# Performance work log

Hardware: AMD Instinct MI355X
Metric: run time of the kernel (lower is better)

Reference implementation:

```python
import jax, jax.numpy as jnp
import numpy as np

VOCAB, XS, HS, NCLASS = 32000, 256, 256, 2
B, DEPTH = 128, 9
NTREE = 2 ** (DEPTH + 1) - 1  # 1023 nodes per perfect binary tree


def setup_inputs() -> dict:
    key = jax.random.key(0)
    ks = jax.random.split(key, 10)
    return {
        'types1': jax.random.randint(ks[0], (B, NTREE), 0, VOCAB, dtype=jnp.int32),
        'types2': jax.random.randint(ks[1], (B, NTREE), 0, VOCAB, dtype=jnp.int32),
        'emb': jax.random.normal(ks[2], (VOCAB, XS), jnp.float32) * 0.1,
        'W_iou': jax.random.normal(ks[3], (3 * HS, XS), jnp.float32) * 0.05,
        'U_iou': jax.random.normal(ks[4], (3 * HS, HS), jnp.float32) * 0.05,
        'b_iou': jnp.zeros((1, 3 * HS), jnp.float32),
        'U_f_w': jax.random.normal(ks[5], (HS, HS), jnp.float32) * 0.05,
        'U_f_b': jnp.zeros((HS,), jnp.float32),
        'cls_w': jax.random.normal(ks[6], (NCLASS, HS), jnp.float32) * 0.05,
        'cls_b': jnp.zeros((NCLASS,), jnp.float32),
    }


def _tree_forward(types, emb, W_iou, U_iou, b_iou, U_f_w, U_f_b):
    # types: [B, NTREE] heap layout (node j has children 2j+1, 2j+2)
    x = emb[types]                       # [B, N, XS] embedding gather
    wx = x @ W_iou.T                     # [B, N, 3H] leaf iou (DGL reduce overwrites it for internal nodes)
    h = jnp.zeros((types.shape[0], NTREE, HS), wx.dtype)
    c = jnp.zeros_like(h)
    for lvl in range(DEPTH, -1, -1):     # bottom-up topological levels (static)
        idx = np.arange(2 ** lvl - 1, 2 ** (lvl + 1) - 1)
        if lvl == DEPTH:  # leaves: no mailbox, keep W_iou(x)
            iou = wx[:, idx] + b_iou
            c_sum = 0.0
        else:
            ch = np.stack([2 * idx + 1, 2 * idx + 2], axis=-1)  # [n, 2]
            h_ch = h[:, ch]              # [B, n, 2, H] child mailbox
            c_ch = c[:, ch]
            h_tild = h_ch.sum(axis=2)
            f = jax.nn.sigmoid(h_ch @ U_f_w.T + U_f_b)
            c_sum = (f * c_ch).sum(axis=2)
            iou = h_tild @ U_iou.T + b_iou  # overwrites wx per DGL semantics
        i, o, u = jnp.split(iou, 3, axis=-1)
        c_new = jax.nn.sigmoid(i) * jnp.tanh(u) + c_sum
        h_new = jax.nn.sigmoid(o) * jnp.tanh(c_new)
        h = h.at[:, idx].set(h_new)
        c = c.at[:, idx].set(c_new)
    return h.mean(axis=1)                # AvgPooling over nodes -> [B, H]


def reference(types1, types2, emb, W_iou, U_iou, b_iou, U_f_w, U_f_b, cls_w, cls_b):
    rep1 = _tree_forward(types1, emb, W_iou, U_iou, b_iou, U_f_w, U_f_b)
    rep2 = _tree_forward(types2, emb, W_iou, U_iou, b_iou, U_f_w, U_f_b)
    return jnp.abs(rep1 - rep2) @ cls_w.T + cls_b  # [B, NCLASS]
```

## Files before the change

kernel.cpp:

```cpp
#include <hip/hip_runtime.h>
#include <math.h>


typedef _Float16 h16;
typedef h16 f16x8 __attribute__((ext_vector_type(8)));
typedef h16 h16x4 __attribute__((ext_vector_type(4)));
typedef float f32x4 __attribute__((ext_vector_type(4)));

#define HS 256
#define NTREE 1023
#define B2 256

#define DMA16(gp, lp) __builtin_amdgcn_global_load_lds( \
    (const __attribute__((address_space(1))) void*)(gp), \
    (__attribute__((address_space(3))) void*)(lp), 16, 0, 0)

__device__ __forceinline__ float sigf(float x){
  return __builtin_amdgcn_rcpf(1.0f + exp2f(x * -1.44269504f));
}
__device__ __forceinline__ float sig_mul_tanh(float a, float b){
  const float E1 = exp2f(a * -1.44269504f);
  const float E2 = exp2f(fminf(b * -2.88539008f, 126.0f));
  return (1.0f - E2) * __builtin_amdgcn_rcpf((1.0f + E1) * (1.0f + E2));
}

__global__ __launch_bounds__(256) void convert_all(const float* __restrict__ emb,
    const float* __restrict__ Ufw, const float* __restrict__ Uiou,
    const float* __restrict__ Wiou, h16* __restrict__ emb16,
    h16* __restrict__ W16, h16* __restrict__ Wx16, float* __restrict__ rep){
  if (blockIdx.x < 64)
    ((float4*)rep)[blockIdx.x*256 + threadIdx.x] = make_float4(0.f,0.f,0.f,0.f);
  const size_t i0 = ((size_t)blockIdx.x*256 + threadIdx.x)*8;
  const float* src; h16* dst; size_t off;
  if (i0 < 8192000UL){ src = emb;  dst = emb16;       off = i0; }
  else if (i0 < 8257536UL){ src = Ufw;  dst = W16;        off = i0 - 8192000UL; }
  else if (i0 < 8454144UL){ src = Uiou; dst = W16+65536;  off = i0 - 8257536UL; }
  else               { src = Wiou; dst = Wx16;       off = i0 - 8454144UL; }
  const float4 v0 = *(const float4*)&src[off];
  const float4 v1 = *(const float4*)&src[off+4];
  f16x8 o;
  o[0]=(h16)v0.x; o[1]=(h16)v0.y; o[2]=(h16)v0.z; o[3]=(h16)v0.w;
  o[4]=(h16)v1.x; o[5]=(h16)v1.y; o[6]=(h16)v1.z; o[7]=(h16)v1.w;
  *(f16x8*)&dst[off] = o;
}

__global__ __launch_bounds__(256) void swizzle_w(const h16* __restrict__ W16,
    h16* __restrict__ Wfrag){
  const int tid = blockIdx.x*256 + threadIdx.x;
  const int lane = tid & 63;
  const int f    = (tid >> 6) & 15;
  const int kc   = (tid >> 10) & 7;
  const int cb   = tid >> 13;
  const int g = f >> 2, cf = f & 3;
  const int row = g*256 + cb*64 + cf*16 + (lane & 15);
  const int col = kc*32 + (lane >> 4)*8;
  const f16x8 v = *(const f16x8*)&W16[(size_t)row*256 + col];
  *(f16x8*)&Wfrag[(size_t)tid*8] = v;
}

__global__ __launch_bounds__(256) void wxv_mfma(const h16* __restrict__ emb16,
    const h16* __restrict__ Wx16, h16* __restrict__ WxV){
  __shared__ h16 As[64*40];
  __shared__ h16 Bs[64*40];
  const int t = threadIdx.x, lane = t & 63, wave = t >> 6;
  const int q = lane >> 4, li = lane & 15;
  const int waveR = wave & 1, waveC = wave >> 1;
  const int bm = blockIdx.x*64, bn = blockIdx.y*64;
  const size_t aAddr = ((size_t)(bm + (t>>2)))*256 + (t&3)*8;
  const size_t bAddr = ((size_t)(bn + (t>>2)))*256 + (t&3)*8;
  const int ldsOff = (t>>2)*40 + (t&3)*8;
  f32x4 acc[2][2] = {};
  for (int k0 = 0; k0 < 256; k0 += 32){
    const f16x8 a = *(const f16x8*)&emb16[aAddr + k0];
    const f16x8 b = *(const f16x8*)&Wx16[bAddr + k0];
    __syncthreads();
    *(f16x8*)&As[ldsOff] = a;
    *(f16x8*)&Bs[ldsOff] = b;
    __syncthreads();
    #pragma unroll
    for (int rt=0; rt<2; ++rt){
      const f16x8 av = *(const f16x8*)&As[(waveR*32 + rt*16 + li)*40 + q*8];
      #pragma unroll
      for (int ct=0; ct<2; ++ct){
        const f16x8 bv = *(const f16x8*)&Bs[(waveC*32 + ct*16 + li)*40 + q*8];
        acc[rt][ct] = __builtin_amdgcn_mfma_f32_16x16x32_f16(av, bv, acc[rt][ct], 0,0,0);
      }
    }
  }
  #pragma unroll
  for (int rt=0; rt<2; ++rt)
    #pragma unroll
    for (int ct=0; ct<2; ++ct){
      const int col = bn + waveC*32 + ct*16 + li;
      #pragma unroll
      for (int reg=0; reg<4; ++reg){
        const int row = bm + waveR*32 + rt*16 + q*4 + reg;
        WxV[(size_t)row*768 + col] = (h16)acc[rt][ct][reg];
      }
    }
}

__global__ __launch_bounds__(256) void type_cell(const h16* __restrict__ WxV,
    const float* __restrict__ biou, h16* __restrict__ hT, h16* __restrict__ cT){
  const int tid = blockIdx.x*256 + threadIdx.x;
  const int row = tid >> 5;
  const int k8  = (tid & 31) * 8;
  const f16x8 vi8 = *(const f16x8*)&WxV[(size_t)row*768 + k8];
  const f16x8 vo8 = *(const f16x8*)&WxV[(size_t)row*768 + 256 + k8];
  const f16x8 vu8 = *(const f16x8*)&WxV[(size_t)row*768 + 512 + k8];
  f16x8 hO, cO;
  #pragma unroll
  for (int j=0; j<8; ++j){
    const float vi = (float)vi8[j] + biou[k8+j];
    const float vo = (float)vo8[j] + biou[256+k8+j];
    const float vu = (float)vu8[j] + biou[512+k8+j];
    const float c = sig_mul_tanh(vi, vu);
    const float h = sig_mul_tanh(vo, c);
    cO[j] = (h16)c; hO[j] = (h16)h;
  }
  *(f16x8*)&hT[(size_t)row*256 + k8] = hO;
  *(f16x8*)&cT[(size_t)row*256 + k8] = cO;
}

__global__ __launch_bounds__(256,3) void gt16_mfma(const h16* __restrict__ hT,
    const h16* __restrict__ Wfrag, const float* __restrict__ biou,
    const float* __restrict__ Ufb, h16* __restrict__ GT16){
  __shared__ h16 ldsA[4*8*64*8];
  __shared__ h16 ldsB[16*64*8];
  const int t = threadIdx.x, w = t >> 6, l = t & 63;
  const int q = l >> 4, li = l & 15;
  const int waveR = w & 1, waveC = w >> 1;
  const int bx = blockIdx.x;

  {
    const int grow = bx*64 + w*16 + li;
    const size_t abase = (size_t)grow * 256;
    #pragma unroll
    for (int kc=0; kc<8; ++kc)
      DMA16(hT + abase + kc*32 + q*8, &ldsA[(w*8 + kc)*512]);
  }

  for (int cb=0; cb<4; ++cb){
    const int colBase = cb*64;
    const h16* wfBase = Wfrag + (size_t)cb*8*16*512 + (size_t)l*8;

    #pragma unroll
    for (int i=0; i<4; ++i)
      DMA16(wfBase + ((size_t)(w*4 + i))*512, &ldsB[(w*4 + i)*512]);
    __syncthreads();

    f32x4 acc[4][2][2] = {};
    #pragma unroll
    for (int kc=0; kc<8; ++kc){
      f16x8 aF[2], bF[4][2];
      #pragma unroll
      for (int rt=0; rt<2; ++rt)
        aF[rt] = *(const f16x8*)&ldsA[(((waveR*2 + rt)*8 + kc)*64 + l)*8];
      #pragma unroll
      for (int g=0; g<4; ++g)
        #pragma unroll
        for (int ct=0; ct<2; ++ct)
          bF[g][ct] = *(const f16x8*)&ldsB[((g*4 + waveC*2 + ct)*64 + l)*8];
      __syncthreads();
      if (kc < 7){
        #pragma unroll
        for (int i=0; i<4; ++i)
          DMA16(wfBase + ((size_t)(kc+1)*16 + w*4 + i)*512,
                &ldsB[(w*4 + i)*512]);
      }
      #pragma unroll
      for (int g=0; g<4; ++g)
        #pragma unroll
        for (int rt=0; rt<2; ++rt)
          #pragma unroll
          for (int ct=0; ct<2; ++ct)
            acc[g][rt][ct] = __builtin_amdgcn_mfma_f32_16x16x32_f16(
                aF[rt], bF[g][ct], acc[g][rt][ct], 0,0,0);
      __syncthreads();
    }

    #pragma unroll
    for (int ct=0; ct<2; ++ct){
      const int c = colBase + waveC*32 + ct*16 + li;
      const float fb  = Ufb[c];
      const float bi2 = 0.5f*biou[c], bo2 = 0.5f*biou[256+c], bu2 = 0.5f*biou[512+c];
      #pragma unroll
      for (int rt=0; rt<2; ++rt){
        #pragma unroll
        for (int reg=0; reg<4; ++reg){
          const int row = bx*64 + waveR*32 + rt*16 + q*4 + reg;
          h16x4 o;
          o[0] = (h16)(acc[0][rt][ct][reg] + fb);
          o[1] = (h16)(acc[1][rt][ct][reg] + bi2);
          o[2] = (h16)(acc[2][rt][ct][reg] + bo2);
          o[3] = (h16)(acc[3][rt][ct][reg] + bu2);
          *(h16x4*)&GT16[(size_t)row*1024 + c*4] = o;
        }
      }
    }
  }
}

__global__ __launch_bounds__(256) void leaf_rep(const int* __restrict__ t1,
    const int* __restrict__ t2, const h16* __restrict__ hT,
    float* __restrict__ rep){
  const int r = blockIdx.y, jg = blockIdx.x, k = threadIdx.x;
  const int* tp = (r < 128) ? t1 : t2;
  const int b = r & 127;
  float s = 0.f;
  for (int jj=0; jj<64; ++jj){
    const int v = tp[b*NTREE + 511 + jg*64 + jj];
    s += (float)hT[(size_t)v*256 + k];
  }
  atomicAdd(&rep[r*HS + k], s);
}

__global__ __launch_bounds__(256) void lvl8_cell(const int* __restrict__ t1,
    const int* __restrict__ t2, const h16* __restrict__ GT16,
    const h16* __restrict__ cT, h16* __restrict__ hUpHigh,
    h16* __restrict__ cPar){
  const int k = threadIdx.x;
  const int m0 = blockIdx.x*32;
  #pragma unroll 4
  for (int p=0; p<32; ++p){
    const int m = m0 + p, rr = m >> 8, jn = m & 255;
    const int* tp = (rr < 128) ? t1 : t2;
    const int b = rr & 127;
    const size_t vl = (size_t)tp[b*NTREE + 511 + 2*jn];
    const size_t vr = (size_t)tp[b*NTREE + 512 + 2*jn];
    const h16x4 gl = *(const h16x4*)&GT16[vl*1024 + k*4];
    const h16x4 gr = *(const h16x4*)&GT16[vr*1024 + k*4];
    const float cl = (float)cT[vl*256 + k];
    const float cr = (float)cT[vr*256 + k];
    const float fl = sigf((float)gl[0]);
    const float fr = sigf((float)gr[0]);
    const float iv = (float)gl[1] + (float)gr[1];
    const float ov = (float)gl[2] + (float)gr[2];
    const float uv = (float)gl[3] + (float)gr[3];
    const float cnew = sig_mul_tanh(iv, uv) + fl*cl + fr*cr;
    const float hnew = sig_mul_tanh(ov, cnew);
    hUpHigh[((size_t)jn*256 + rr)*256 + k] = (h16)hnew;
    cPar[(size_t)m*256 + k] = (h16)cnew;
  }
}

__global__ __launch_bounds__(256,3) void level_mfma(
    const h16* __restrict__ hChild, const h16* __restrict__ cChild,
    const h16* __restrict__ Wfrag,
    const float* __restrict__ biou, const float* __restrict__ Ufb,
    h16* __restrict__ hUpW, h16* __restrict__ cPar,
    int log2n, int cbN, int cOff, int ndOff){
  const int n = 1 << log2n;
  const int mask2 = 2*n - 1;
  __shared__ h16 ldsA[4*8*64*8];
  __shared__ h16 ldsB[16*64*8];
  const int t = threadIdx.x, w = t >> 6, l = t & 63;
  const int q = l >> 4, li = l & 15;
  const int waveR = w & 1, waveC = w >> 1;
  const int bx = blockIdx.x;

  {
    const int grow = bx*64 + w*16 + li;
    const int cidx = grow & mask2;
    const int rr   = grow >> (log2n + 1);
    const size_t abase = ((size_t)(cOff + cidx)*256 + rr)*256;
    #pragma unroll
    for (int kc=0; kc<8; ++kc)
      DMA16(hChild + abase + kc*32 + q*8, &ldsA[(w*8 + kc)*512]);
  }

  for (int cb=0; cb<cbN; ++cb){
    const int cbi = blockIdx.y*cbN + cb;
    const int colBase = cbi*64;
    const h16* wfBase = Wfrag + (size_t)cbi*8*16*512 + (size_t)l*8;

    #pragma unroll
    for (int i=0; i<4; ++i)
      DMA16(wfBase + ((size_t)(w*4 + i))*512, &ldsB[(w*4 + i)*512]);
    __syncthreads();

    f32x4 acc[4][2][2] = {};
    #pragma unroll
    for (int kc=0; kc<8; ++kc){
      f16x8 aF[2], bF[4][2];
      #pragma unroll
      for (int rt=0; rt<2; ++rt)
        aF[rt] = *(const f16x8*)&ldsA[(((waveR*2 + rt)*8 + kc)*64 + l)*8];
      #pragma unroll
      for (int g=0; g<4; ++g)
        #pragma unroll
        for (int ct=0; ct<2; ++ct)
          bF[g][ct] = *(const f16x8*)&ldsB[((g*4 + waveC*2 + ct)*64 + l)*8];
      __syncthreads();
      if (kc < 7){
        #pragma unroll
        for (int i=0; i<4; ++i)
          DMA16(wfBase + ((size_t)(kc+1)*16 + w*4 + i)*512,
                &ldsB[(w*4 + i)*512]);
      }
      #pragma unroll
      for (int g=0; g<4; ++g)
        #pragma unroll
        for (int rt=0; rt<2; ++rt)
          #pragma unroll
          for (int ct=0; ct<2; ++ct)
            acc[g][rt][ct] = __builtin_amdgcn_mfma_f32_16x16x32_f16(
                aF[rt], bF[g][ct], acc[g][rt][ct], 0,0,0);
      __syncthreads();
    }

    #pragma unroll
    for (int ct=0; ct<2; ++ct){
      const int c = colBase + waveC*32 + ct*16 + li;
      const float fb  = Ufb[c];
      const float bi_ = biou[c], bo_ = biou[256+c], bu_ = biou[512+c];
      #pragma unroll
      for (int rt=0; rt<2; ++rt){
        #pragma unroll
        for (int pp=0; pp<2; ++pp){
          const int crel = waveR*32 + rt*16 + q*4 + 2*pp;
          const int m = bx*32 + (crel >> 1);
          const int rr2 = m >> log2n;
          const int jn = m & (n - 1);
          const float cl = (float)cChild[(size_t)(bx*64 + crel)*256 + c];
          const float cr = (float)cChild[(size_t)(bx*64 + crel + 1)*256 + c];
          const float fl = sigf(acc[0][rt][ct][2*pp]   + fb);
          const float fr = sigf(acc[0][rt][ct][2*pp+1] + fb);
          const float iv = acc[1][rt][ct][2*pp] + acc[1][rt][ct][2*pp+1] + bi_;
          const float ov = acc[2][rt][ct][2*pp] + acc[2][rt][ct][2*pp+1] + bo_;
          const float uv = acc[3][rt][ct][2*pp] + acc[3][rt][ct][2*pp+1] + bu_;
          const float cnew = sig_mul_tanh(iv, uv) + fl*cl + fr*cr;
          const float hnew = sig_mul_tanh(ov, cnew);
          hUpW[(((size_t)(ndOff + jn))*256 + rr2)*256 + c] = (h16)hnew;
          cPar[((size_t)m)*256 + c] = (h16)cnew;
        }
      }
    }
  }
}

__global__ __launch_bounds__(256) void rep_accum(const h16* __restrict__ H,
    float* __restrict__ rep, int nrows, int chunk){
  const int r = blockIdx.y, k = threadIdx.x;
  const int n0 = blockIdx.x * chunk;
  int n1 = n0 + chunk; if (n1 > nrows) n1 = nrows;
  float s = 0.f;
  for (int nd = n0; nd < n1; ++nd)
    s += (float)H[((size_t)nd*256 + r)*HS + k];
  atomicAdd(&rep[r*HS + k], s);
}

__global__ __launch_bounds__(256) void cls_kernel(const float* __restrict__ rep,
    const float* __restrict__ clsw, const float* __restrict__ clsb,
    float* __restrict__ out){
  const int b = blockIdx.x, k = threadIdx.x;
  const float d = fabsf(rep[b*HS + k] - rep[(128+b)*HS + k]) * (1.0f/1023.0f);
  __shared__ float r0[256], r1[256];
  r0[k] = d * clsw[k];
  r1[k] = d * clsw[HS + k];
  __syncthreads();
  for (int off = 128; off > 0; off >>= 1){
    if (k < off){ r0[k] += r0[k+off]; r1[k] += r1[k+off]; }
    __syncthreads();
  }
  if (k == 0){
    out[b*2 + 0] = r0[0] + clsb[0];
    out[b*2 + 1] = r1[0] + clsb[1];
  }
}

extern "C" void kernel_launch(void* const* d_in, const int* in_sizes, int n_in,
                              void* d_out, int out_size, void* d_ws, size_t ws_size,
                              hipStream_t stream){
  const int*   types1 = (const int*)d_in[0];
  const int*   types2 = (const int*)d_in[1];
  const float* emb    = (const float*)d_in[2];
  const float* Wiou   = (const float*)d_in[3];
  const float* Uiou   = (const float*)d_in[4];
  const float* biou   = (const float*)d_in[5];
  const float* Ufw    = (const float*)d_in[6];
  const float* Ufb    = (const float*)d_in[7];
  const float* clsw   = (const float*)d_in[8];
  const float* clsb   = (const float*)d_in[9];
  float* out = (float*)d_out;

  h16* ws      = (h16*)d_ws;
  h16* GT16    = ws;
  h16* WxV     = ws;
  h16* emb16   = ws + 24576000UL;
  h16* Wx16    = ws + 32768000UL;
  h16* hUpLow  = ws;
  h16* cB      = ws + 16711680UL;
  h16* hT      = ws + 65536000UL;
  h16* cT      = ws + 73728000UL;
  h16* hUpHigh = ws + 81920000UL;
  h16* cA      = ws + 98697216UL;
  h16* W16     = ws + 115474432UL;
  h16* Wfrag   = ws + 115736576UL;
  float* rep   = (float*)(ws + 116260864UL);

  convert_all<<<4224, 256, 0, stream>>>(emb, Ufw, Uiou, Wiou, emb16, W16, Wx16, rep);
  swizzle_w<<<256, 256, 0, stream>>>(W16, Wfrag);
  wxv_mfma<<<dim3(500,12), 256, 0, stream>>>(emb16, Wx16, WxV);
  type_cell<<<4000, 256, 0, stream>>>(WxV, biou, hT, cT);
  gt16_mfma<<<500, 256, 0, stream>>>(hT, Wfrag, biou, Ufb, GT16);
  leaf_rep<<<dim3(8, B2), 256, 0, stream>>>(types1, types2, hT, rep);
  lvl8_cell<<<2048, 256, 0, stream>>>(types1, types2, GT16, cT, hUpHigh, cA);

  const h16* cprev = cA;
  for (int lvl = 7; lvl >= 0; --lvl){
    const int children = 512 << lvl;
    const int cbN = (lvl >= 6) ? 4 : 1;
    h16* cout = ((8 - lvl) & 1) ? cB : cA;
    const h16* hin = (lvl == 7) ? hUpHigh : hUpLow;
    const int cOff  = (lvl == 7) ? 0 : ((1 << (lvl + 1)) - 1);
    const int ndOff = (1 << lvl) - 1;
    level_mfma<<<dim3(children/64, 4/cbN), 256, 0, stream>>>(
        hin, cprev, Wfrag, biou, Ufb, hUpLow, cout,
        lvl, cbN, cOff, ndOff);
    cprev = cout;
  }
  rep_accum<<<dim3(2, B2), 256, 0, stream>>>(hUpLow,  rep, 255, 128);
  rep_accum<<<dim3(2, B2), 256, 0, stream>>>(hUpHigh, rep, 256, 128);
  cls_kernel<<<128, 256, 0, stream>>>(rep, clsw, clsb, out);
}
```

Before: 475.2 us.

## Fuse leaf GEMM with LSTM cell, fold leaf pooling into level-8 kernel

```diff
diff --git a/kernel.cpp b/kernel.cpp
--- a/kernel.cpp
+++ b/kernel.cpp
@@ -44,82 +44,112 @@
   *(f16x8*)&dst[off] = o;
 }
 
-__global__ __launch_bounds__(256) void swizzle_w(const h16* __restrict__ W16,
-    h16* __restrict__ Wfrag){
+__global__ __launch_bounds__(256) void swizzle_all(const h16* __restrict__ W16,
+    const h16* __restrict__ Wx16, h16* __restrict__ Wfrag,
+    h16* __restrict__ WxFrag){
   const int tid = blockIdx.x*256 + threadIdx.x;
-  const int lane = tid & 63;
-  const int f    = (tid >> 6) & 15;
-  const int kc   = (tid >> 10) & 7;
-  const int cb   = tid >> 13;
-  const int g = f >> 2, cf = f & 3;
-  const int row = g*256 + cb*64 + cf*16 + (lane & 15);
-  const int col = kc*32 + (lane >> 4)*8;
-  const f16x8 v = *(const f16x8*)&W16[(size_t)row*256 + col];
-  *(f16x8*)&Wfrag[(size_t)tid*8] = v;
-}
-
-__global__ __launch_bounds__(256) void wxv_mfma(const h16* __restrict__ emb16,
-    const h16* __restrict__ Wx16, h16* __restrict__ WxV){
-  __shared__ h16 As[64*40];
-  __shared__ h16 Bs[64*40];
-  const int t = threadIdx.x, lane = t & 63, wave = t >> 6;
-  const int q = lane >> 4, li = lane & 15;
-  const int waveR = wave & 1, waveC = wave >> 1;
-  const int bm = blockIdx.x*64, bn = blockIdx.y*64;
-  const size_t aAddr = ((size_t)(bm + (t>>2)))*256 + (t&3)*8;
-  const size_t bAddr = ((size_t)(bn + (t>>2)))*256 + (t&3)*8;
-  const int ldsOff = (t>>2)*40 + (t&3)*8;
-  f32x4 acc[2][2] = {};
-  for (int k0 = 0; k0 < 256; k0 += 32){
-    const f16x8 a = *(const f16x8*)&emb16[aAddr + k0];
-    const f16x8 b = *(const f16x8*)&Wx16[bAddr + k0];
+  if (tid < 65536){
+    const int lane = tid & 63;
+    const int f    = (tid >> 6) & 15;
+    const int kc   = (tid >> 10) & 7;
+    const int cb   = tid >> 13;
+    const int g = f >> 2, cf = f & 3;
+    const int row = g*256 + cb*64 + cf*16 + (lane & 15);
+    const int col = kc*32 + (lane >> 4)*8;
+    const f16x8 v = *(const f16x8*)&W16[(size_t)row*256 + col];
+    *(f16x8*)&Wfrag[(size_t)tid*8] = v;
+  } else {
+    const int t2 = tid - 65536;
+    const int lane = t2 & 63;
+    const int frag = t2 >> 6;
+    const int cb  = frag / 96;
+    const int rem = frag % 96;
+    const int kc  = rem / 12;
+    const int f   = rem % 12;
+    const int g = f >> 2, cf = f & 3;
+    const int row = g*256 + cb*64 + cf*16 + (lane & 15);
+    const int col = kc*32 + (lane >> 4)*8;
+    const f16x8 v = *(const f16x8*)&Wx16[(size_t)row*256 + col];
+    *(f16x8*)&WxFrag[(size_t)frag*512 + lane*8] = v;
+  }
+}
+
+__global__ __launch_bounds__(256,3) void ht_mfma(const h16* __restrict__ emb16,
+    const h16* __restrict__ WxFrag, const float* __restrict__ biou,
+    h16* __restrict__ hT, h16* __restrict__ cT){
+  __shared__ h16 ldsA[4*8*64*8];
+  __shared__ h16 ldsB[12*64*8];
+  const int t = threadIdx.x, w = t >> 6, l = t & 63;
+  const int q = l >> 4, li = l & 15;
+  const int waveR = w & 1, waveC = w >> 1;
+  const int bx = blockIdx.x;
+
+  {
+    const int grow = bx*64 + w*16 + li;
+    const size_t abase = (size_t)grow * 256;
+    #pragma unroll
+    for (int kc=0; kc<8; ++kc)
+      DMA16(emb16 + abase + kc*32 + q*8, &ldsA[(w*8 + kc)*512]);
+  }
+
+  for (int cb=0; cb<4; ++cb){
+    const h16* wfBase = WxFrag + (size_t)cb*8*12*512 + (size_t)l*8;
+
+    #pragma unroll
+    for (int i=0; i<3; ++i)
+      DMA16(wfBase + ((size_t)(w*3 + i))*512, &ldsB[(w*3 + i)*512]);
     __syncthreads();
-    *(f16x8*)&As[ldsOff] = a;
-    *(f16x8*)&Bs[ldsOff] = b;
-    __syncthreads();
-    #pragma unroll
-    for (int rt=0; rt<2; ++rt){
-      const f16x8 av = *(const f16x8*)&As[(waveR*32 + rt*16 + li)*40 + q*8];
-      #pragma unroll
-      for (int ct=0; ct<2; ++ct){
-        const f16x8 bv = *(const f16x8*)&Bs[(waveC*32 + ct*16 + li)*40 + q*8];
-        acc[rt][ct] = __builtin_amdgcn_mfma_f32_16x16x32_f16(av, bv, acc[rt][ct], 0,0,0);
-      }
-    }
-  }
-  #pragma unroll
-  for (int rt=0; rt<2; ++rt)
+
+    f32x4 acc[3][2][2] = {};
+    #pragma unroll
+    for (int kc=0; kc<8; ++kc){
+      f16x8 aF[2], bF[3][2];
+      #pragma unroll
+      for (int rt=0; rt<2; ++rt)
+        aF[rt] = *(const f16x8*)&ldsA[(((waveR*2 + rt)*8 + kc)*64 + l)*8];
+      #pragma unroll
+      for (int g=0; g<3; ++g)
+        #pragma unroll
+        for (int ct=0; ct<2; ++ct)
+          bF[g][ct] = *(const f16x8*)&ldsB[((g*4 + waveC*2 + ct)*64 + l)*8];
+      __syncthreads();
+      if (kc < 7){
+        #pragma unroll
+        for (int i=0; i<3; ++i)
+          DMA16(wfBase + ((size_t)(kc+1)*12 + w*3 + i)*512,
+                &ldsB[(w*3 + i)*512]);
+      }
+      #pragma unroll
+      for (int g=0; g<3; ++g)
+        #pragma unroll
+        for (int rt=0; rt<2; ++rt)
+          #pragma unroll
+          for (int ct=0; ct<2; ++ct)
+            acc[g][rt][ct] = __builtin_amdgcn_mfma_f32_16x16x32_f16(
+                aF[rt], bF[g][ct], acc[g][rt][ct], 0,0,0);
+      __syncthreads();
+    }
+
     #pragma unroll
     for (int ct=0; ct<2; ++ct){
-      const int col = bn + waveC*32 + ct*16 + li;
-      #pragma unroll
-      for (int reg=0; reg<4; ++reg){
-        const int row = bm + waveR*32 + rt*16 + q*4 + reg;
-        WxV[(size_t)row*768 + col] = (h16)acc[rt][ct][reg];
-      }
-    }
-}
-
-__global__ __launch_bounds__(256) void type_cell(const h16* __restrict__ WxV,
-    const float* __restrict__ biou, h16* __restrict__ hT, h16* __restrict__ cT){
-  const int tid = blockIdx.x*256 + threadIdx.x;
-  const int row = tid >> 5;
-  const int k8  = (tid & 31) * 8;
-  const f16x8 vi8 = *(const f16x8*)&WxV[(size_t)row*768 + k8];
-  const f16x8 vo8 = *(const f16x8*)&WxV[(size_t)row*768 + 256 + k8];
-  const f16x8 vu8 = *(const f16x8*)&WxV[(size_t)row*768 + 512 + k8];
-  f16x8 hO, cO;
-  #pragma unroll
-  for (int j=0; j<8; ++j){
-    const float vi = (float)vi8[j] + biou[k8+j];
-    const float vo = (float)vo8[j] + biou[256+k8+j];
-    const float vu = (float)vu8[j] + biou[512+k8+j];
-    const float c = sig_mul_tanh(vi, vu);
-    const float h = sig_mul_tanh(vo, c);
-    cO[j] = (h16)c; hO[j] = (h16)h;
-  }
-  *(f16x8*)&hT[(size_t)row*256 + k8] = hO;
-  *(f16x8*)&cT[(size_t)row*256 + k8] = cO;
+      const int c = cb*64 + waveC*32 + ct*16 + li;
+      const float bi = biou[c], bo = biou[256+c], bu = biou[512+c];
+      #pragma unroll
+      for (int rt=0; rt<2; ++rt){
+        #pragma unroll
+        for (int reg=0; reg<4; ++reg){
+          const int row = bx*64 + waveR*32 + rt*16 + q*4 + reg;
+          const float iv = acc[0][rt][ct][reg] + bi;
+          const float ov = acc[1][rt][ct][reg] + bo;
+          const float uv = acc[2][rt][ct][reg] + bu;
+          const float cc = sig_mul_tanh(iv, uv);
+          const float hh = sig_mul_tanh(ov, cc);
+          hT[(size_t)row*256 + c] = (h16)hh;
+          cT[(size_t)row*256 + c] = (h16)cc;
+        }
+      }
+    }
+  }
 }
 
 __global__ __launch_bounds__(256,3) void gt16_mfma(const h16* __restrict__ hT,
@@ -141,7 +171,6 @@
   }
 
   for (int cb=0; cb<4; ++cb){
-    const int colBase = cb*64;
     const h16* wfBase = Wfrag + (size_t)cb*8*16*512 + (size_t)l*8;
 
     #pragma unroll
@@ -181,7 +210,7 @@
 
     #pragma unroll
     for (int ct=0; ct<2; ++ct){
-      const int c = colBase + waveC*32 + ct*16 + li;
+      const int c = cb*64 + waveC*32 + ct*16 + li;
       const float fb  = Ufb[c];
       const float bi2 = 0.5f*biou[c], bo2 = 0.5f*biou[256+c], bu2 = 0.5f*biou[512+c];
       #pragma unroll
@@ -201,31 +230,20 @@
   }
 }
 
-__global__ __launch_bounds__(256) void leaf_rep(const int* __restrict__ t1,
-    const int* __restrict__ t2, const h16* __restrict__ hT,
-    float* __restrict__ rep){
-  const int r = blockIdx.y, jg = blockIdx.x, k = threadIdx.x;
-  const int* tp = (r < 128) ? t1 : t2;
-  const int b = r & 127;
-  float s = 0.f;
-  for (int jj=0; jj<64; ++jj){
-    const int v = tp[b*NTREE + 511 + jg*64 + jj];
-    s += (float)hT[(size_t)v*256 + k];
-  }
-  atomicAdd(&rep[r*HS + k], s);
-}
-
 __global__ __launch_bounds__(256) void lvl8_cell(const int* __restrict__ t1,
     const int* __restrict__ t2, const h16* __restrict__ GT16,
-    const h16* __restrict__ cT, h16* __restrict__ hUpHigh,
-    h16* __restrict__ cPar){
+    const h16* __restrict__ cT, const h16* __restrict__ hT,
+    h16* __restrict__ hUpHigh, h16* __restrict__ cPar,
+    float* __restrict__ rep){
   const int k = threadIdx.x;
   const int m0 = blockIdx.x*32;
+  const int rr = m0 >> 8;
+  const int* tp = (rr < 128) ? t1 : t2;
+  const int b = rr & 127;
+  float s = 0.f;
   #pragma unroll 4
   for (int p=0; p<32; ++p){
-    const int m = m0 + p, rr = m >> 8, jn = m & 255;
-    const int* tp = (rr < 128) ? t1 : t2;
-    const int b = rr & 127;
+    const int m = m0 + p, jn = m & 255;
     const size_t vl = (size_t)tp[b*NTREE + 511 + 2*jn];
     const size_t vr = (size_t)tp[b*NTREE + 512 + 2*jn];
     const h16x4 gl = *(const h16x4*)&GT16[vl*1024 + k*4];
@@ -241,7 +259,9 @@
     const float hnew = sig_mul_tanh(ov, cnew);
     hUpHigh[((size_t)jn*256 + rr)*256 + k] = (h16)hnew;
     cPar[(size_t)m*256 + k] = (h16)cnew;
-  }
+    s += (float)hT[vl*256 + k] + (float)hT[vr*256 + k];
+  }
+  atomicAdd(&rep[rr*HS + k], s);
 }
 
 __global__ __launch_bounds__(256,3) void level_mfma(
@@ -386,7 +406,6 @@
 
   h16* ws      = (h16*)d_ws;
   h16* GT16    = ws;
-  h16* WxV     = ws;
   h16* emb16   = ws + 24576000UL;
   h16* Wx16    = ws + 32768000UL;
   h16* hUpLow  = ws;
@@ -398,19 +417,19 @@
   h16* W16     = ws + 115474432UL;
   h16* Wfrag   = ws + 115736576UL;
   float* rep   = (float*)(ws + 116260864UL);
+  h16* WxFrag  = ws + 116391936UL;
 
   convert_all<<<4224, 256, 0, stream>>>(emb, Ufw, Uiou, Wiou, emb16, W16, Wx16, rep);
-  swizzle_w<<<256, 256, 0, stream>>>(W16, Wfrag);
-  wxv_mfma<<<dim3(500,12), 256, 0, stream>>>(emb16, Wx16, WxV);
-  type_cell<<<4000, 256, 0, stream>>>(WxV, biou, hT, cT);
+  swizzle_all<<<352, 256, 0, stream>>>(W16, Wx16, Wfrag, WxFrag);
+  ht_mfma<<<500, 256, 0, stream>>>(emb16, WxFrag, biou, hT, cT);
   gt16_mfma<<<500, 256, 0, stream>>>(hT, Wfrag, biou, Ufb, GT16);
-  leaf_rep<<<dim3(8, B2), 256, 0, stream>>>(types1, types2, hT, rep);
-  lvl8_cell<<<2048, 256, 0, stream>>>(types1, types2, GT16, cT, hUpHigh, cA);
+  lvl8_cell<<<2048, 256, 0, stream>>>(types1, types2, GT16, cT, hT,
+                                      hUpHigh, cA, rep);
 
   const h16* cprev = cA;
   for (int lvl = 7; lvl >= 0; --lvl){
     const int children = 512 << lvl;
-    const int cbN = (lvl >= 6) ? 4 : 1;
+    const int cbN = (lvl == 7) ? 2 : ((lvl == 6) ? 4 : 1);
     h16* cout = ((8 - lvl) & 1) ? cB : cA;
     const h16* hin = (lvl == 7) ? hUpHigh : hUpLow;
     const int cOff  = (lvl == 7) ? 0 : ((1 << (lvl + 1)) - 1);
```

New measurement: 449.5 us. 5.4% less time.
